# Performance work log

Hardware: AMD Instinct MI355X
Metric: run time of the kernel (lower is better)

## Reference

```python
import jax, jax.numpy as jnp
import numpy as np

N_NODES = 100000
N_EDGES = 1600000
D_IN = 256
H = 4       # n_heads
F = 64      # out_feats per head
NEG_SLOPE = 0.2


def setup_inputs() -> dict:
    key = jax.random.key(0)
    ks = jax.random.split(key, 8)
    feat = jax.random.normal(ks[0], (N_NODES, D_IN), dtype=jnp.float32)
    src = jax.random.randint(ks[1], (N_EDGES,), 0, N_NODES, dtype=jnp.int32)
    dst = jnp.sort(jax.random.randint(ks[2], (N_EDGES,), 0, N_NODES, dtype=jnp.int32))
    s = 1.0 / np.sqrt(D_IN)
    W_src = jax.random.normal(ks[3], (D_IN, H * F), dtype=jnp.float32) * s
    W_dst = jax.random.normal(ks[4], (D_IN, H * F), dtype=jnp.float32) * s
    b_dst = jnp.zeros((H * F,), dtype=jnp.float32)
    Wa_src = jax.random.normal(ks[5], (D_IN, H), dtype=jnp.float32) * s
    Wa_dst = jax.random.normal(ks[6], (D_IN, H), dtype=jnp.float32) * s
    return {"feat": feat, "W_src": W_src, "W_dst": W_dst, "b_dst": b_dst,
            "Wa_src": Wa_src, "Wa_dst": Wa_dst, "src": src, "dst": dst}


def reference(feat, W_src, W_dst, b_dst, Wa_src, Wa_dst, src, dst):
    N = feat.shape[0]
    # node projections
    h_src = (feat @ W_src).reshape(N, H, F)                  # [N,H,F]
    h_dst = (feat @ W_dst + b_dst).reshape(N, H, F)          # residual term
    a_src = feat @ Wa_src                                    # [N,H]
    a_dst = feat @ Wa_dst                                    # [N,H]
    # per-edge attention logits: u_add_v then leaky_relu
    e = a_src[src] + a_dst[dst]                              # [E,H]
    e = jnp.where(e > 0, e, NEG_SLOPE * e)
    # edge softmax grouped by destination node
    emax = jax.ops.segment_max(e, dst, num_segments=N)       # [N,H]
    emax = jnp.where(jnp.isfinite(emax), emax, 0.0)          # empty segments -> 0
    ex = jnp.exp(e - emax[dst])                              # [E,H]
    denom = jax.ops.segment_sum(ex, dst, num_segments=N)     # [N,H]
    a = ex / denom[dst]                                      # [E,H]
    # u_mul_e + sum aggregation
    msg = h_src[src] * a[:, :, None]                         # [E,H,F]
    out = jax.ops.segment_sum(msg, dst, num_segments=N)      # [N,H,F]
    return out + h_dst
```

## Files before the change

### kernel.cpp

```cpp
#include <hip/hip_runtime.h>

#define N_NODES 100000
#define N_EDGES 1600000
#define NEG_SLOPE 0.2f

typedef __bf16 bf16x8 __attribute__((ext_vector_type(8)));
typedef float f32x4 __attribute__((ext_vector_type(4)));

__device__ inline unsigned short f2bf(float f) {
    union { float f; unsigned u; } x; x.f = f;
    unsigned r = x.u + 0x7fffu + ((x.u >> 16) & 1u);
    return (unsigned short)(r >> 16);
}
__device__ inline float rlanef(float v, int l) {
    union { float f; int i; } x; x.f = v;
    x.i = __builtin_amdgcn_readlane(x.i, l);
    return x.f;
}

__global__ __launch_bounds__(256) void cvt_w_k(const float* __restrict__ Ws,
                                               const float* __restrict__ Wd,
                                               unsigned short* __restrict__ Wsw_src,
                                               unsigned short* __restrict__ Wsw_dst) {
    int idx = blockIdx.x * 256 + threadIdx.x;
    int sel = idx >> 16;
    int r = idx & 65535;
    int k = r >> 8, n = r & 255;
    int ct = n >> 4, nl = n & 15;
    int lane = ((k & 31) >> 3) * 16 + nl, j = k & 7;
    int ks = k >> 5;
    unsigned short v = f2bf((sel == 0 ? Ws : Wd)[k * 256 + n]);
    (sel == 0 ? Wsw_src : Wsw_dst)[(ct * 8 + ks) * 512 + lane * 8 + j] = v;
}

__global__ void cvt_wa_k(const float* __restrict__ Was,
                         const float* __restrict__ Wad,
                         unsigned short* __restrict__ Wa_sw) {
    int idx = blockIdx.x * 256 + threadIdx.x;
    int j = idx & 7, lane = (idx >> 3) & 63, ks = idx >> 9;
    int n = lane & 15, k = ks * 32 + (lane >> 4) * 8 + j;
    float v = n < 4 ? Was[k * 4 + n] : (n < 8 ? Wad[k * 4 + (n - 4)] : 0.f);
    Wa_sw[idx] = f2bf(v);
}

__global__ __launch_bounds__(256) void aproj_k(const float* __restrict__ feat,
                                               const unsigned short* __restrict__ Wa_sw,
                                               float* __restrict__ a_src,
                                               float* __restrict__ a_dst) {
    int wave = threadIdx.x >> 6, lane = threadIdx.x & 63;
    int quad = lane >> 4, l16 = lane & 15;
    int row_strip = (blockIdx.x * 4 + wave) * 16;
    int arow = row_strip + l16;
    if (arow >= N_NODES) arow = N_NODES - 1;
    const float* arow_p = feat + (size_t)arow * 256;
    const bf16x8* Wa8 = (const bf16x8*)Wa_sw;
    f32x4 acc = {0.f, 0.f, 0.f, 0.f};
    #pragma unroll
    for (int ks = 0; ks < 8; ++ks) {
        int k0 = ks * 32 + quad * 8;
        float4 f0 = *(const float4*)(arow_p + k0);
        float4 f1 = *(const float4*)(arow_p + k0 + 4);
        union { unsigned short u[8]; bf16x8 v; } cv;
        cv.u[0] = f2bf(f0.x); cv.u[1] = f2bf(f0.y);
        cv.u[2] = f2bf(f0.z); cv.u[3] = f2bf(f0.w);
        cv.u[4] = f2bf(f1.x); cv.u[5] = f2bf(f1.y);
        cv.u[6] = f2bf(f1.z); cv.u[7] = f2bf(f1.w);
        acc = __builtin_amdgcn_mfma_f32_16x16x32_bf16(cv.v, Wa8[ks * 64 + lane], acc, 0, 0, 0);
    }
    #pragma unroll
    for (int r = 0; r < 4; ++r) {
        int n = row_strip + quad * 4 + r;
        if (n < N_NODES) {
            if (l16 < 4)      a_src[n * 4 + l16] = acc[r];
            else if (l16 < 8) a_dst[n * 4 + (l16 - 4)] = acc[r];
        }
    }
}

__global__ void rowptr_k(const int* __restrict__ dst, int* __restrict__ rp) {
    int n = blockIdx.x * 256 + threadIdx.x;
    if (n > N_NODES) return;
    int lo = 0, hi = N_EDGES;
    while (lo < hi) { int mid = (lo + hi) >> 1; if (dst[mid] < n) lo = mid + 1; else hi = mid; }
    rp[n] = lo;
}

__global__ __launch_bounds__(512, 6) void agg_k(const int* __restrict__ src,
                                                const int* __restrict__ rp,
                                                const float* __restrict__ a_src,
                                                const float* __restrict__ a_dst,
                                                const float* __restrict__ feat,
                                                const unsigned short* __restrict__ Wsw_src,
                                                const unsigned short* __restrict__ Wsw_dst,
                                                const float* __restrict__ b_dst,
                                                float* __restrict__ out) {
    __shared__ unsigned short G[4 * 32 * 17 * 8];
    __shared__ unsigned short F[32 * 17 * 8];
    int tid = threadIdx.x, wave = tid >> 6, lane = tid & 63;
    int base = blockIdx.x * 16;

    #pragma unroll
    for (int e = tid; e < 1024; e += 512) {
        int m = e >> 6, k0 = (e & 63) * 4;
        float4 f = *(const float4*)(feat + (size_t)(base + m) * 256 + k0);
        ushort4 u;
        u.x = f2bf(f.x); u.y = f2bf(f.y); u.z = f2bf(f.z); u.w = f2bf(f.w);
        int ks = k0 >> 5, quad = (k0 >> 3) & 3, jb = k0 & 7;
        *(ushort4*)&F[((ks * 4 + quad) * 17 + m) * 8 + jb] = u;
    }

    for (int i = 0; i < 2; ++i) {
        int m = wave * 2 + i;
        int node = base + m;
        int r0 = rp[node], r1 = rp[node + 1];
        int deg = r1 - r0;
        f32x4 g0 = {0.f,0.f,0.f,0.f}, g1 = g0, g2 = g0, g3 = g0;

        if (deg > 0 && deg <= 64) {
            float4 adv = *(const float4*)(a_dst + node * 4);
            bool act = lane < deg;
            int s = 0;
            float4 av = {0.f, 0.f, 0.f, 0.f};
            if (act) {
                s = src[r0 + lane];
                av = *(const float4*)(a_src + s * 4);
            }
            float e0 = av.x + adv.x; e0 = e0 > 0.f ? e0 : NEG_SLOPE * e0;
            float e1 = av.y + adv.y; e1 = e1 > 0.f ? e1 : NEG_SLOPE * e1;
            float e2 = av.z + adv.z; e2 = e2 > 0.f ? e2 : NEG_SLOPE * e2;
            float e3 = av.w + adv.w; e3 = e3 > 0.f ? e3 : NEG_SLOPE * e3;
            if (!act) { e0 = e1 = e2 = e3 = -1e30f; }
            float m0 = e0, m1 = e1, m2 = e2, m3 = e3;
            #pragma unroll
            for (int off = 32; off > 0; off >>= 1) {
                m0 = fmaxf(m0, __shfl_xor(m0, off));
                m1 = fmaxf(m1, __shfl_xor(m1, off));
                m2 = fmaxf(m2, __shfl_xor(m2, off));
                m3 = fmaxf(m3, __shfl_xor(m3, off));
            }
            float w0 = act ? __expf(e0 - m0) : 0.f;
            float w1 = act ? __expf(e1 - m1) : 0.f;
            float w2 = act ? __expf(e2 - m2) : 0.f;
            float w3 = act ? __expf(e3 - m3) : 0.f;
            float d0 = w0, d1 = w1, d2 = w2, d3 = w3;
            #pragma unroll
            for (int off = 32; off > 0; off >>= 1) {
                d0 += __shfl_xor(d0, off); d1 += __shfl_xor(d1, off);
                d2 += __shfl_xor(d2, off); d3 += __shfl_xor(d3, off);
            }
            w0 *= 1.f / d0; w1 *= 1.f / d1; w2 *= 1.f / d2; w3 *= 1.f / d3;
            int j = 0;
            for (; j + 4 <= deg; j += 4) {
                int s0 = __builtin_amdgcn_readlane(s, j);
                int s1 = __builtin_amdgcn_readlane(s, j + 1);
                int s2 = __builtin_amdgcn_readlane(s, j + 2);
                int s3 = __builtin_amdgcn_readlane(s, j + 3);
                f32x4 f0 = *(const f32x4*)(feat + (size_t)s0 * 256 + lane * 4);
                f32x4 f1 = *(const f32x4*)(feat + (size_t)s1 * 256 + lane * 4);
                f32x4 f2 = *(const f32x4*)(feat + (size_t)s2 * 256 + lane * 4);
                f32x4 f3 = *(const f32x4*)(feat + (size_t)s3 * 256 + lane * 4);
                float a0 = rlanef(w0, j),   b0 = rlanef(w1, j),   c0 = rlanef(w2, j),   x0 = rlanef(w3, j);
                float a1 = rlanef(w0, j+1), b1 = rlanef(w1, j+1), c1 = rlanef(w2, j+1), x1 = rlanef(w3, j+1);
                float a2 = rlanef(w0, j+2), b2 = rlanef(w1, j+2), c2 = rlanef(w2, j+2), x2 = rlanef(w3, j+2);
                float a3 = rlanef(w0, j+3), b3 = rlanef(w1, j+3), c3 = rlanef(w2, j+3), x3 = rlanef(w3, j+3);
                g0 += a0 * f0; g1 += b0 * f0; g2 += c0 * f0; g3 += x0 * f0;
                g0 += a1 * f1; g1 += b1 * f1; g2 += c1 * f1; g3 += x1 * f1;
                g0 += a2 * f2; g1 += b2 * f2; g2 += c2 * f2; g3 += x2 * f2;
                g0 += a3 * f3; g1 += b3 * f3; g2 += c3 * f3; g3 += x3 * f3;
            }
            for (; j < deg; ++j) {
                int sj   = __builtin_amdgcn_readlane(s, j);
                float wx = rlanef(w0, j), wy = rlanef(w1, j);
                float wz = rlanef(w2, j), ww = rlanef(w3, j);
                f32x4 f = *(const f32x4*)(feat + (size_t)sj * 256 + lane * 4);
                g0 += wx * f; g1 += wy * f; g2 += wz * f; g3 += ww * f;
            }
        } else if (deg > 64) {
            float4 adv = *(const float4*)(a_dst + node * 4);
            float m0 = -1e30f, m1 = -1e30f, m2 = -1e30f, m3 = -1e30f;
            for (int e = r0 + lane; e < r1; e += 64) {
                int s = src[e];
                float4 av = *(const float4*)(a_src + s * 4);
                float e0 = av.x + adv.x; e0 = e0 > 0.f ? e0 : NEG_SLOPE * e0;
                float e1 = av.y + adv.y; e1 = e1 > 0.f ? e1 : NEG_SLOPE * e1;
                float e2 = av.z + adv.z; e2 = e2 > 0.f ? e2 : NEG_SLOPE * e2;
                float e3 = av.w + adv.w; e3 = e3 > 0.f ? e3 : NEG_SLOPE * e3;
                m0 = fmaxf(m0, e0); m1 = fmaxf(m1, e1);
                m2 = fmaxf(m2, e2); m3 = fmaxf(m3, e3);
            }
            #pragma unroll
            for (int off = 32; off > 0; off >>= 1) {
                m0 = fmaxf(m0, __shfl_xor(m0, off));
                m1 = fmaxf(m1, __shfl_xor(m1, off));
                m2 = fmaxf(m2, __shfl_xor(m2, off));
                m3 = fmaxf(m3, __shfl_xor(m3, off));
            }
            float d0 = 0.f, d1 = 0.f, d2 = 0.f, d3 = 0.f;
            for (int e = r0 + lane; e < r1; e += 64) {
                int s = src[e];
                float4 av = *(const float4*)(a_src + s * 4);
                float e0 = av.x + adv.x; e0 = e0 > 0.f ? e0 : NEG_SLOPE * e0;
                float e1 = av.y + adv.y; e1 = e1 > 0.f ? e1 : NEG_SLOPE * e1;
                float e2 = av.z + adv.z; e2 = e2 > 0.f ? e2 : NEG_SLOPE * e2;
                float e3 = av.w + adv.w; e3 = e3 > 0.f ? e3 : NEG_SLOPE * e3;
                d0 += __expf(e0 - m0); d1 += __expf(e1 - m1);
                d2 += __expf(e2 - m2); d3 += __expf(e3 - m3);
            }
            #pragma unroll
            for (int off = 32; off > 0; off >>= 1) {
                d0 += __shfl_xor(d0, off); d1 += __shfl_xor(d1, off);
                d2 += __shfl_xor(d2, off); d3 += __shfl_xor(d3, off);
            }
            float i0 = 1.f / d0, i1 = 1.f / d1, i2 = 1.f / d2, i3 = 1.f / d3;
            for (int c0 = r0; c0 < r1; c0 += 64) {
                int cnt = min(64, r1 - c0);
                int s = 0; float w0 = 0.f, w1 = 0.f, w2 = 0.f, w3 = 0.f;
                if (lane < cnt) {
                    s = src[c0 + lane];
                    float4 av = *(const float4*)(a_src + s * 4);
                    float e0 = av.x + adv.x; e0 = e0 > 0.f ? e0 : NEG_SLOPE * e0;
                    float e1 = av.y + adv.y; e1 = e1 > 0.f ? e1 : NEG_SLOPE * e1;
                    float e2 = av.z + adv.z; e2 = e2 > 0.f ? e2 : NEG_SLOPE * e2;
                    float e3 = av.w + adv.w; e3 = e3 > 0.f ? e3 : NEG_SLOPE * e3;
                    w0 = __expf(e0 - m0) * i0; w1 = __expf(e1 - m1) * i1;
                    w2 = __expf(e2 - m2) * i2; w3 = __expf(e3 - m3) * i3;
                }
                for (int j = 0; j < cnt; ++j) {
                    int sj   = __builtin_amdgcn_readlane(s, j);
                    float wx = rlanef(w0, j), wy = rlanef(w1, j);
                    float wz = rlanef(w2, j), ww = rlanef(w3, j);
                    f32x4 f = *(const f32x4*)(feat + (size_t)sj * 256 + lane * 4);
                    g0 += wx * f; g1 += wy * f; g2 += wz * f; g3 += ww * f;
                }
            }
        }

        int g8 = lane >> 1, off4 = (lane & 1) * 4;
        ushort4 u;
        u.x = f2bf(g0[0]); u.y = f2bf(g0[1]); u.z = f2bf(g0[2]); u.w = f2bf(g0[3]);
        *(ushort4*)&G[((0 * 32 + g8) * 17 + m) * 8 + off4] = u;
        u.x = f2bf(g1[0]); u.y = f2bf(g1[1]); u.z = f2bf(g1[2]); u.w = f2bf(g1[3]);
        *(ushort4*)&G[((1 * 32 + g8) * 17 + m) * 8 + off4] = u;
        u.x = f2bf(g2[0]); u.y = f2bf(g2[1]); u.z = f2bf(g2[2]); u.w = f2bf(g2[3]);
        *(ushort4*)&G[((2 * 32 + g8) * 17 + m) * 8 + off4] = u;
        u.x = f2bf(g3[0]); u.y = f2bf(g3[1]); u.z = f2bf(g3[2]); u.w = f2bf(g3[3]);
        *(ushort4*)&G[((3 * 32 + g8) * 17 + m) * 8 + off4] = u;
    }
    __syncthreads();

    int h = wave >> 1, hc = (wave & 1) * 2;
    int quad = lane >> 4, l16 = lane & 15;
    f32x4 acc[2];
    acc[0] = (f32x4){0.f, 0.f, 0.f, 0.f};
    acc[1] = (f32x4){0.f, 0.f, 0.f, 0.f};
    const bf16x8* Ws8 = (const bf16x8*)Wsw_src;
    const bf16x8* Wd8 = (const bf16x8*)Wsw_dst;
    #pragma unroll
    for (int ks = 0; ks < 8; ++ks) {
        bf16x8 a1 = *(const bf16x8*)&G[((h * 32 + ks * 4 + quad) * 17 + l16) * 8];
        bf16x8 a2 = *(const bf16x8*)&F[((ks * 4 + quad) * 17 + l16) * 8];
        #pragma unroll
        for (int c = 0; c < 2; ++c) {
            int ct = hc + c;
            acc[c] = __builtin_amdgcn_mfma_f32_16x16x32_bf16(
                a1, Ws8[((h * 4 + ct) * 8 + ks) * 64 + lane], acc[c], 0, 0, 0);
            acc[c] = __builtin_amdgcn_mfma_f32_16x16x32_bf16(
                a2, Wd8[((h * 4 + ct) * 8 + ks) * 64 + lane], acc[c], 0, 0, 0);
        }
    }
    #pragma unroll
    for (int c = 0; c < 2; ++c) {
        int col = h * 64 + (hc + c) * 16 + l16;
        float b = b_dst[col];
        #pragma unroll
        for (int r = 0; r < 4; ++r)
            out[(size_t)(base + quad * 4 + r) * 256 + col] = acc[c][r] + b;
    }
}

extern "C" void kernel_launch(void* const* d_in, const int* in_sizes, int n_in,
                              void* d_out, int out_size, void* d_ws, size_t ws_size,
                              hipStream_t stream) {
    const float* feat   = (const float*)d_in[0];
    const float* W_src  = (const float*)d_in[1];
    const float* W_dst  = (const float*)d_in[2];
    const float* b_dst  = (const float*)d_in[3];
    const float* Wa_src = (const float*)d_in[4];
    const float* Wa_dst = (const float*)d_in[5];
    const int*   src    = (const int*)d_in[6];
    const int*   dst    = (const int*)d_in[7];
    float* out = (float*)d_out;

    char* ws = (char*)d_ws;
    unsigned short* Wsw_src = (unsigned short*)(ws);
    unsigned short* Wsw_dst = (unsigned short*)(ws + 131072);
    unsigned short* Wa_sw   = (unsigned short*)(ws + 262144);
    float* a_src            = (float*)(ws + 270336);
    float* a_dst            = (float*)(ws + 1870336);
    int*   rp               = (int*)(ws + 3470336);

    hipLaunchKernelGGL(cvt_w_k,  dim3(512),  dim3(256), 0, stream, W_src, W_dst, Wsw_src, Wsw_dst);
    hipLaunchKernelGGL(cvt_wa_k, dim3(16),   dim3(256), 0, stream, Wa_src, Wa_dst, Wa_sw);
    hipLaunchKernelGGL(aproj_k,  dim3(1563), dim3(256), 0, stream, feat, Wa_sw, a_src, a_dst);
    hipLaunchKernelGGL(rowptr_k, dim3(391),  dim3(256), 0, stream, dst, rp);
    hipLaunchKernelGGL(agg_k,    dim3(6250), dim3(512), 0, stream, src, rp, a_src, a_dst,
                       feat, Wsw_src, Wsw_dst, b_dst, out);
}
```

Baseline: 469.6 us.

## Project features before aggregation and gather fp16 h_src instead of raw feat

Splits the fused gather-then-project kernel into a dense projection kernel, which writes h_src in fp16 and the h_dst+bias residual into out, followed by an aggregation kernel with one wave per node. Each edge now gathers 256 fp16 values (512 B) instead of 256 fp32 feat values (1 KB), and does a single weighted sum per lane rather than four per-head sums. Attention logits are stored as fp16, softmax weights are passed through shared memory instead of readlane, and the shuffle reductions stop once they cover the node's degree. The cost is an extra 51 MB round trip for h_src plus a read-modify-write of out, along with some precision loss from fp16 storage.

```diff
diff --git a/kernel.cpp b/kernel.cpp
--- a/kernel.cpp
+++ b/kernel.cpp
@@ -6,16 +6,12 @@
 
 typedef __bf16 bf16x8 __attribute__((ext_vector_type(8)));
 typedef float f32x4 __attribute__((ext_vector_type(4)));
+typedef _Float16 f16x4 __attribute__((ext_vector_type(4)));
 
 __device__ inline unsigned short f2bf(float f) {
     union { float f; unsigned u; } x; x.f = f;
     unsigned r = x.u + 0x7fffu + ((x.u >> 16) & 1u);
     return (unsigned short)(r >> 16);
-}
-__device__ inline float rlanef(float v, int l) {
-    union { float f; int i; } x; x.f = v;
-    x.i = __builtin_amdgcn_readlane(x.i, l);
-    return x.f;
 }
 
 __global__ __launch_bounds__(256) void cvt_w_k(const float* __restrict__ Ws,
@@ -43,10 +39,18 @@
     Wa_sw[idx] = f2bf(v);
 }
 
+__global__ void rowptr_k(const int* __restrict__ dst, int* __restrict__ rp) {
+    int n = blockIdx.x * 256 + threadIdx.x;
+    if (n > N_NODES) return;
+    int lo = 0, hi = N_EDGES;
+    while (lo < hi) { int mid = (lo + hi) >> 1; if (dst[mid] < n) lo = mid + 1; else hi = mid; }
+    rp[n] = lo;
+}
+
 __global__ __launch_bounds__(256) void aproj_k(const float* __restrict__ feat,
                                                const unsigned short* __restrict__ Wa_sw,
-                                               float* __restrict__ a_src,
-                                               float* __restrict__ a_dst) {
+                                               _Float16* __restrict__ a_srcH,
+                                               _Float16* __restrict__ a_dstH) {
     int wave = threadIdx.x >> 6, lane = threadIdx.x & 63;
     int quad = lane >> 4, l16 = lane & 15;
     int row_strip = (blockIdx.x * 4 + wave) * 16;
@@ -71,211 +75,241 @@
     for (int r = 0; r < 4; ++r) {
         int n = row_strip + quad * 4 + r;
         if (n < N_NODES) {
-            if (l16 < 4)      a_src[n * 4 + l16] = acc[r];
-            else if (l16 < 8) a_dst[n * 4 + (l16 - 4)] = acc[r];
-        }
-    }
-}
-
-__global__ void rowptr_k(const int* __restrict__ dst, int* __restrict__ rp) {
-    int n = blockIdx.x * 256 + threadIdx.x;
-    if (n > N_NODES) return;
-    int lo = 0, hi = N_EDGES;
-    while (lo < hi) { int mid = (lo + hi) >> 1; if (dst[mid] < n) lo = mid + 1; else hi = mid; }
-    rp[n] = lo;
-}
-
-__global__ __launch_bounds__(512, 6) void agg_k(const int* __restrict__ src,
-                                                const int* __restrict__ rp,
-                                                const float* __restrict__ a_src,
-                                                const float* __restrict__ a_dst,
-                                                const float* __restrict__ feat,
-                                                const unsigned short* __restrict__ Wsw_src,
-                                                const unsigned short* __restrict__ Wsw_dst,
-                                                const float* __restrict__ b_dst,
-                                                float* __restrict__ out) {
-    __shared__ unsigned short G[4 * 32 * 17 * 8];
-    __shared__ unsigned short F[32 * 17 * 8];
+            if (l16 < 4)      a_srcH[(size_t)n * 4 + l16] = (_Float16)acc[r];
+            else if (l16 < 8) a_dstH[(size_t)n * 4 + (l16 - 4)] = (_Float16)acc[r];
+        }
+    }
+}
+
+__global__ __launch_bounds__(512) void proj_k(const float* __restrict__ feat,
+                                              const unsigned short* __restrict__ Wsw_src,
+                                              const unsigned short* __restrict__ Wsw_dst,
+                                              const float* __restrict__ b_dst,
+                                              _Float16* __restrict__ h_src,
+                                              float* __restrict__ out) {
+    __shared__ unsigned short F[4 * 32 * 17 * 8];
     int tid = threadIdx.x, wave = tid >> 6, lane = tid & 63;
-    int base = blockIdx.x * 16;
-
-    #pragma unroll
-    for (int e = tid; e < 1024; e += 512) {
-        int m = e >> 6, k0 = (e & 63) * 4;
-        float4 f = *(const float4*)(feat + (size_t)(base + m) * 256 + k0);
+    int quad = lane >> 4, l16 = lane & 15;
+    int base = blockIdx.x * 64;
+
+    #pragma unroll
+    for (int it = 0; it < 8; ++it) {
+        int c = tid + it * 512;
+        int m = c >> 6, k0 = (c & 63) * 4;
+        int row = base + m; if (row > N_NODES - 1) row = N_NODES - 1;
+        float4 f = *(const float4*)(feat + (size_t)row * 256 + k0);
         ushort4 u;
         u.x = f2bf(f.x); u.y = f2bf(f.y); u.z = f2bf(f.z); u.w = f2bf(f.w);
-        int ks = k0 >> 5, quad = (k0 >> 3) & 3, jb = k0 & 7;
-        *(ushort4*)&F[((ks * 4 + quad) * 17 + m) * 8 + jb] = u;
-    }
-
-    for (int i = 0; i < 2; ++i) {
-        int m = wave * 2 + i;
-        int node = base + m;
-        int r0 = rp[node], r1 = rp[node + 1];
-        int deg = r1 - r0;
-        f32x4 g0 = {0.f,0.f,0.f,0.f}, g1 = g0, g2 = g0, g3 = g0;
-
-        if (deg > 0 && deg <= 64) {
-            float4 adv = *(const float4*)(a_dst + node * 4);
-            bool act = lane < deg;
-            int s = 0;
-            float4 av = {0.f, 0.f, 0.f, 0.f};
-            if (act) {
-                s = src[r0 + lane];
-                av = *(const float4*)(a_src + s * 4);
-            }
-            float e0 = av.x + adv.x; e0 = e0 > 0.f ? e0 : NEG_SLOPE * e0;
-            float e1 = av.y + adv.y; e1 = e1 > 0.f ? e1 : NEG_SLOPE * e1;
-            float e2 = av.z + adv.z; e2 = e2 > 0.f ? e2 : NEG_SLOPE * e2;
-            float e3 = av.w + adv.w; e3 = e3 > 0.f ? e3 : NEG_SLOPE * e3;
-            if (!act) { e0 = e1 = e2 = e3 = -1e30f; }
-            float m0 = e0, m1 = e1, m2 = e2, m3 = e3;
+        int strip = m >> 4, ms = m & 15, kq = k0 >> 3, jb = k0 & 7;
+        *(ushort4*)&F[((strip * 32 + kq) * 17 + ms) * 8 + jb] = u;
+    }
+    __syncthreads();
+
+    bool isSrc = wave < 4;
+    int cg = (wave & 3) * 4;
+    const bf16x8* W8 = (const bf16x8*)(isSrc ? Wsw_src : Wsw_dst);
+
+    f32x4 acc[4][4];
+    #pragma unroll
+    for (int s = 0; s < 4; ++s)
+        #pragma unroll
+        for (int c = 0; c < 4; ++c) acc[s][c] = (f32x4){0.f, 0.f, 0.f, 0.f};
+
+    #pragma unroll
+    for (int ks = 0; ks < 8; ++ks) {
+        bf16x8 B0 = W8[((cg + 0) * 8 + ks) * 64 + lane];
+        bf16x8 B1 = W8[((cg + 1) * 8 + ks) * 64 + lane];
+        bf16x8 B2 = W8[((cg + 2) * 8 + ks) * 64 + lane];
+        bf16x8 B3 = W8[((cg + 3) * 8 + ks) * 64 + lane];
+        #pragma unroll
+        for (int s = 0; s < 4; ++s) {
+            bf16x8 A = *(const bf16x8*)&F[((s * 32 + ks * 4 + quad) * 17 + l16) * 8];
+            acc[s][0] = __builtin_amdgcn_mfma_f32_16x16x32_bf16(A, B0, acc[s][0], 0, 0, 0);
+            acc[s][1] = __builtin_amdgcn_mfma_f32_16x16x32_bf16(A, B1, acc[s][1], 0, 0, 0);
+            acc[s][2] = __builtin_amdgcn_mfma_f32_16x16x32_bf16(A, B2, acc[s][2], 0, 0, 0);
+            acc[s][3] = __builtin_amdgcn_mfma_f32_16x16x32_bf16(A, B3, acc[s][3], 0, 0, 0);
+        }
+    }
+
+    if (isSrc) {
+        #pragma unroll
+        for (int s = 0; s < 4; ++s)
             #pragma unroll
-            for (int off = 32; off > 0; off >>= 1) {
-                m0 = fmaxf(m0, __shfl_xor(m0, off));
-                m1 = fmaxf(m1, __shfl_xor(m1, off));
-                m2 = fmaxf(m2, __shfl_xor(m2, off));
-                m3 = fmaxf(m3, __shfl_xor(m3, off));
-            }
-            float w0 = act ? __expf(e0 - m0) : 0.f;
-            float w1 = act ? __expf(e1 - m1) : 0.f;
-            float w2 = act ? __expf(e2 - m2) : 0.f;
-            float w3 = act ? __expf(e3 - m3) : 0.f;
-            float d0 = w0, d1 = w1, d2 = w2, d3 = w3;
-            #pragma unroll
-            for (int off = 32; off > 0; off >>= 1) {
-                d0 += __shfl_xor(d0, off); d1 += __shfl_xor(d1, off);
-                d2 += __shfl_xor(d2, off); d3 += __shfl_xor(d3, off);
-            }
-            w0 *= 1.f / d0; w1 *= 1.f / d1; w2 *= 1.f / d2; w3 *= 1.f / d3;
-            int j = 0;
-            for (; j + 4 <= deg; j += 4) {
-                int s0 = __builtin_amdgcn_readlane(s, j);
-                int s1 = __builtin_amdgcn_readlane(s, j + 1);
-                int s2 = __builtin_amdgcn_readlane(s, j + 2);
-                int s3 = __builtin_amdgcn_readlane(s, j + 3);
-                f32x4 f0 = *(const f32x4*)(feat + (size_t)s0 * 256 + lane * 4);
-                f32x4 f1 = *(const f32x4*)(feat + (size_t)s1 * 256 + lane * 4);
-                f32x4 f2 = *(const f32x4*)(feat + (size_t)s2 * 256 + lane * 4);
-                f32x4 f3 = *(const f32x4*)(feat + (size_t)s3 * 256 + lane * 4);
-                float a0 = rlanef(w0, j),   b0 = rlanef(w1, j),   c0 = rlanef(w2, j),   x0 = rlanef(w3, j);
-                float a1 = rlanef(w0, j+1), b1 = rlanef(w1, j+1), c1 = rlanef(w2, j+1), x1 = rlanef(w3, j+1);
-                float a2 = rlanef(w0, j+2), b2 = rlanef(w1, j+2), c2 = rlanef(w2, j+2), x2 = rlanef(w3, j+2);
-                float a3 = rlanef(w0, j+3), b3 = rlanef(w1, j+3), c3 = rlanef(w2, j+3), x3 = rlanef(w3, j+3);
-                g0 += a0 * f0; g1 += b0 * f0; g2 += c0 * f0; g3 += x0 * f0;
-                g0 += a1 * f1; g1 += b1 * f1; g2 += c1 * f1; g3 += x1 * f1;
-                g0 += a2 * f2; g1 += b2 * f2; g2 += c2 * f2; g3 += x2 * f2;
-                g0 += a3 * f3; g1 += b3 * f3; g2 += c3 * f3; g3 += x3 * f3;
-            }
-            for (; j < deg; ++j) {
-                int sj   = __builtin_amdgcn_readlane(s, j);
-                float wx = rlanef(w0, j), wy = rlanef(w1, j);
-                float wz = rlanef(w2, j), ww = rlanef(w3, j);
-                f32x4 f = *(const f32x4*)(feat + (size_t)sj * 256 + lane * 4);
-                g0 += wx * f; g1 += wy * f; g2 += wz * f; g3 += ww * f;
-            }
-        } else if (deg > 64) {
-            float4 adv = *(const float4*)(a_dst + node * 4);
-            float m0 = -1e30f, m1 = -1e30f, m2 = -1e30f, m3 = -1e30f;
-            for (int e = r0 + lane; e < r1; e += 64) {
-                int s = src[e];
-                float4 av = *(const float4*)(a_src + s * 4);
-                float e0 = av.x + adv.x; e0 = e0 > 0.f ? e0 : NEG_SLOPE * e0;
-                float e1 = av.y + adv.y; e1 = e1 > 0.f ? e1 : NEG_SLOPE * e1;
-                float e2 = av.z + adv.z; e2 = e2 > 0.f ? e2 : NEG_SLOPE * e2;
-                float e3 = av.w + adv.w; e3 = e3 > 0.f ? e3 : NEG_SLOPE * e3;
-                m0 = fmaxf(m0, e0); m1 = fmaxf(m1, e1);
-                m2 = fmaxf(m2, e2); m3 = fmaxf(m3, e3);
-            }
-            #pragma unroll
-            for (int off = 32; off > 0; off >>= 1) {
-                m0 = fmaxf(m0, __shfl_xor(m0, off));
-                m1 = fmaxf(m1, __shfl_xor(m1, off));
-                m2 = fmaxf(m2, __shfl_xor(m2, off));
-                m3 = fmaxf(m3, __shfl_xor(m3, off));
-            }
-            float d0 = 0.f, d1 = 0.f, d2 = 0.f, d3 = 0.f;
-            for (int e = r0 + lane; e < r1; e += 64) {
-                int s = src[e];
-                float4 av = *(const float4*)(a_src + s * 4);
-                float e0 = av.x + adv.x; e0 = e0 > 0.f ? e0 : NEG_SLOPE * e0;
-                float e1 = av.y + adv.y; e1 = e1 > 0.f ? e1 : NEG_SLOPE * e1;
-                float e2 = av.z + adv.z; e2 = e2 > 0.f ? e2 : NEG_SLOPE * e2;
-                float e3 = av.w + adv.w; e3 = e3 > 0.f ? e3 : NEG_SLOPE * e3;
-                d0 += __expf(e0 - m0); d1 += __expf(e1 - m1);
-                d2 += __expf(e2 - m2); d3 += __expf(e3 - m3);
-            }
-            #pragma unroll
-            for (int off = 32; off > 0; off >>= 1) {
-                d0 += __shfl_xor(d0, off); d1 += __shfl_xor(d1, off);
-                d2 += __shfl_xor(d2, off); d3 += __shfl_xor(d3, off);
-            }
-            float i0 = 1.f / d0, i1 = 1.f / d1, i2 = 1.f / d2, i3 = 1.f / d3;
-            for (int c0 = r0; c0 < r1; c0 += 64) {
-                int cnt = min(64, r1 - c0);
-                int s = 0; float w0 = 0.f, w1 = 0.f, w2 = 0.f, w3 = 0.f;
-                if (lane < cnt) {
-                    s = src[c0 + lane];
-                    float4 av = *(const float4*)(a_src + s * 4);
-                    float e0 = av.x + adv.x; e0 = e0 > 0.f ? e0 : NEG_SLOPE * e0;
-                    float e1 = av.y + adv.y; e1 = e1 > 0.f ? e1 : NEG_SLOPE * e1;
-                    float e2 = av.z + adv.z; e2 = e2 > 0.f ? e2 : NEG_SLOPE * e2;
-                    float e3 = av.w + adv.w; e3 = e3 > 0.f ? e3 : NEG_SLOPE * e3;
-                    w0 = __expf(e0 - m0) * i0; w1 = __expf(e1 - m1) * i1;
-                    w2 = __expf(e2 - m2) * i2; w3 = __expf(e3 - m3) * i3;
-                }
-                for (int j = 0; j < cnt; ++j) {
-                    int sj   = __builtin_amdgcn_readlane(s, j);
-                    float wx = rlanef(w0, j), wy = rlanef(w1, j);
-                    float wz = rlanef(w2, j), ww = rlanef(w3, j);
-                    f32x4 f = *(const f32x4*)(feat + (size_t)sj * 256 + lane * 4);
-                    g0 += wx * f; g1 += wy * f; g2 += wz * f; g3 += ww * f;
+            for (int c = 0; c < 4; ++c) {
+                int col = (cg + c) * 16 + l16;
+                #pragma unroll
+                for (int r = 0; r < 4; ++r) {
+                    int row = base + s * 16 + quad * 4 + r;
+                    if (row < N_NODES)
+                        h_src[(size_t)row * 256 + col] = (_Float16)acc[s][c][r];
                 }
             }
-        }
-
-        int g8 = lane >> 1, off4 = (lane & 1) * 4;
-        ushort4 u;
-        u.x = f2bf(g0[0]); u.y = f2bf(g0[1]); u.z = f2bf(g0[2]); u.w = f2bf(g0[3]);
-        *(ushort4*)&G[((0 * 32 + g8) * 17 + m) * 8 + off4] = u;
-        u.x = f2bf(g1[0]); u.y = f2bf(g1[1]); u.z = f2bf(g1[2]); u.w = f2bf(g1[3]);
-        *(ushort4*)&G[((1 * 32 + g8) * 17 + m) * 8 + off4] = u;
-        u.x = f2bf(g2[0]); u.y = f2bf(g2[1]); u.z = f2bf(g2[2]); u.w = f2bf(g2[3]);
-        *(ushort4*)&G[((2 * 32 + g8) * 17 + m) * 8 + off4] = u;
-        u.x = f2bf(g3[0]); u.y = f2bf(g3[1]); u.z = f2bf(g3[2]); u.w = f2bf(g3[3]);
-        *(ushort4*)&G[((3 * 32 + g8) * 17 + m) * 8 + off4] = u;
-    }
-    __syncthreads();
-
-    int h = wave >> 1, hc = (wave & 1) * 2;
-    int quad = lane >> 4, l16 = lane & 15;
-    f32x4 acc[2];
-    acc[0] = (f32x4){0.f, 0.f, 0.f, 0.f};
-    acc[1] = (f32x4){0.f, 0.f, 0.f, 0.f};
-    const bf16x8* Ws8 = (const bf16x8*)Wsw_src;
-    const bf16x8* Wd8 = (const bf16x8*)Wsw_dst;
-    #pragma unroll
-    for (int ks = 0; ks < 8; ++ks) {
-        bf16x8 a1 = *(const bf16x8*)&G[((h * 32 + ks * 4 + quad) * 17 + l16) * 8];
-        bf16x8 a2 = *(const bf16x8*)&F[((ks * 4 + quad) * 17 + l16) * 8];
-        #pragma unroll
-        for (int c = 0; c < 2; ++c) {
-            int ct = hc + c;
-            acc[c] = __builtin_amdgcn_mfma_f32_16x16x32_bf16(
-                a1, Ws8[((h * 4 + ct) * 8 + ks) * 64 + lane], acc[c], 0, 0, 0);
-            acc[c] = __builtin_amdgcn_mfma_f32_16x16x32_bf16(
-                a2, Wd8[((h * 4 + ct) * 8 + ks) * 64 + lane], acc[c], 0, 0, 0);
-        }
-    }
-    #pragma unroll
-    for (int c = 0; c < 2; ++c) {
-        int col = h * 64 + (hc + c) * 16 + l16;
-        float b = b_dst[col];
-        #pragma unroll
-        for (int r = 0; r < 4; ++r)
-            out[(size_t)(base + quad * 4 + r) * 256 + col] = acc[c][r] + b;
-    }
+    } else {
+        #pragma unroll
+        for (int c = 0; c < 4; ++c) {
+            int col = (cg + c) * 16 + l16;
+            float b = b_dst[col];
+            #pragma unroll
+            for (int s = 0; s < 4; ++s)
+                #pragma unroll
+                for (int r = 0; r < 4; ++r) {
+                    int row = base + s * 16 + quad * 4 + r;
+                    if (row < N_NODES)
+                        out[(size_t)row * 256 + col] = acc[s][c][r] + b;
+                }
+        }
+    }
+}
+
+__global__ __launch_bounds__(256, 6) void agg2_k(const int* __restrict__ src,
+                                                 const int* __restrict__ rp,
+                                                 const _Float16* __restrict__ a_srcH,
+                                                 const _Float16* __restrict__ a_dstH,
+                                                 const _Float16* __restrict__ h_src,
+                                                 float* __restrict__ out) {
+    __shared__ float WT[4][64][4];
+    int tid = threadIdx.x, wave = tid >> 6, lane = tid & 63;
+    int node = blockIdx.x * 4 + wave;
+    int head = lane >> 4;
+    int r0 = rp[node], r1 = rp[node + 1], deg = r1 - r0;
+
+    size_t o = (size_t)node * 256 + lane * 4;
+    float4 pv = *(const float4*)(out + o);
+
+    f32x4 g = (f32x4){0.f, 0.f, 0.f, 0.f};
+    const _Float16* hl = h_src + lane * 4;
+
+    if (deg > 0 && deg <= 64) {
+        f16x4 adv4 = *(const f16x4*)(a_dstH + (size_t)node * 4);
+        float ad0 = (float)adv4[0], ad1 = (float)adv4[1];
+        float ad2 = (float)adv4[2], ad3 = (float)adv4[3];
+        bool act = lane < deg;
+        int s = 0;
+        f16x4 av4 = (f16x4){0, 0, 0, 0};
+        if (act) {
+            s = src[r0 + lane];
+            av4 = *(const f16x4*)(a_srcH + (size_t)s * 4);
+        }
+        float e0 = (float)av4[0] + ad0; e0 = e0 > 0.f ? e0 : NEG_SLOPE * e0;
+        float e1 = (float)av4[1] + ad1; e1 = e1 > 0.f ? e1 : NEG_SLOPE * e1;
+        float e2 = (float)av4[2] + ad2; e2 = e2 > 0.f ? e2 : NEG_SLOPE * e2;
+        float e3 = (float)av4[3] + ad3; e3 = e3 > 0.f ? e3 : NEG_SLOPE * e3;
+        if (!act) { e0 = e1 = e2 = e3 = -1e30f; }
+        float m0 = e0, m1 = e1, m2 = e2, m3 = e3;
+        for (int off = 1; off < deg; off <<= 1) {
+            m0 = fmaxf(m0, __shfl_xor(m0, off));
+            m1 = fmaxf(m1, __shfl_xor(m1, off));
+            m2 = fmaxf(m2, __shfl_xor(m2, off));
+            m3 = fmaxf(m3, __shfl_xor(m3, off));
+        }
+        float w0 = act ? __expf(e0 - m0) : 0.f;
+        float w1 = act ? __expf(e1 - m1) : 0.f;
+        float w2 = act ? __expf(e2 - m2) : 0.f;
+        float w3 = act ? __expf(e3 - m3) : 0.f;
+        float d0 = w0, d1 = w1, d2 = w2, d3 = w3;
+        for (int off = 1; off < deg; off <<= 1) {
+            d0 += __shfl_xor(d0, off); d1 += __shfl_xor(d1, off);
+            d2 += __shfl_xor(d2, off); d3 += __shfl_xor(d3, off);
+        }
+        w0 *= 1.f / d0; w1 *= 1.f / d1; w2 *= 1.f / d2; w3 *= 1.f / d3;
+        float4 wv; wv.x = w0; wv.y = w1; wv.z = w2; wv.w = w3;
+        *(float4*)&WT[wave][lane][0] = wv;
+        asm volatile("s_waitcnt lgkmcnt(0)" ::: "memory");
+
+        int j = 0;
+        for (; j + 4 <= deg; j += 4) {
+            int s0 = __builtin_amdgcn_readlane(s, j);
+            int s1 = __builtin_amdgcn_readlane(s, j + 1);
+            int s2 = __builtin_amdgcn_readlane(s, j + 2);
+            int s3 = __builtin_amdgcn_readlane(s, j + 3);
+            f16x4 h0 = *(const f16x4*)(hl + (size_t)s0 * 256);
+            f16x4 h1 = *(const f16x4*)(hl + (size_t)s1 * 256);
+            f16x4 h2 = *(const f16x4*)(hl + (size_t)s2 * 256);
+            f16x4 h3 = *(const f16x4*)(hl + (size_t)s3 * 256);
+            float x0 = WT[wave][j][head],     x1 = WT[wave][j + 1][head];
+            float x2 = WT[wave][j + 2][head], x3 = WT[wave][j + 3][head];
+            g[0] += x0 * (float)h0[0]; g[1] += x0 * (float)h0[1];
+            g[2] += x0 * (float)h0[2]; g[3] += x0 * (float)h0[3];
+            g[0] += x1 * (float)h1[0]; g[1] += x1 * (float)h1[1];
+            g[2] += x1 * (float)h1[2]; g[3] += x1 * (float)h1[3];
+            g[0] += x2 * (float)h2[0]; g[1] += x2 * (float)h2[1];
+            g[2] += x2 * (float)h2[2]; g[3] += x2 * (float)h2[3];
+            g[0] += x3 * (float)h3[0]; g[1] += x3 * (float)h3[1];
+            g[2] += x3 * (float)h3[2]; g[3] += x3 * (float)h3[3];
+        }
+        for (; j < deg; ++j) {
+            int sj = __builtin_amdgcn_readlane(s, j);
+            float xj = WT[wave][j][head];
+            f16x4 h = *(const f16x4*)(hl + (size_t)sj * 256);
+            g[0] += xj * (float)h[0]; g[1] += xj * (float)h[1];
+            g[2] += xj * (float)h[2]; g[3] += xj * (float)h[3];
+        }
+    } else if (deg > 64) {
+        f16x4 adv4 = *(const f16x4*)(a_dstH + (size_t)node * 4);
+        float ad0 = (float)adv4[0], ad1 = (float)adv4[1];
+        float ad2 = (float)adv4[2], ad3 = (float)adv4[3];
+        float m0 = -1e30f, m1 = -1e30f, m2 = -1e30f, m3 = -1e30f;
+        for (int e = r0 + lane; e < r1; e += 64) {
+            int se = src[e];
+            f16x4 av4 = *(const f16x4*)(a_srcH + (size_t)se * 4);
+            float e0 = (float)av4[0] + ad0; e0 = e0 > 0.f ? e0 : NEG_SLOPE * e0;
+            float e1 = (float)av4[1] + ad1; e1 = e1 > 0.f ? e1 : NEG_SLOPE * e1;
+            float e2 = (float)av4[2] + ad2; e2 = e2 > 0.f ? e2 : NEG_SLOPE * e2;
+            float e3 = (float)av4[3] + ad3; e3 = e3 > 0.f ? e3 : NEG_SLOPE * e3;
+            m0 = fmaxf(m0, e0); m1 = fmaxf(m1, e1);
+            m2 = fmaxf(m2, e2); m3 = fmaxf(m3, e3);
+        }
+        #pragma unroll
+        for (int off = 32; off > 0; off >>= 1) {
+            m0 = fmaxf(m0, __shfl_xor(m0, off)); m1 = fmaxf(m1, __shfl_xor(m1, off));
+            m2 = fmaxf(m2, __shfl_xor(m2, off)); m3 = fmaxf(m3, __shfl_xor(m3, off));
+        }
+        float d0 = 0.f, d1 = 0.f, d2 = 0.f, d3 = 0.f;
+        for (int e = r0 + lane; e < r1; e += 64) {
+            int se = src[e];
+            f16x4 av4 = *(const f16x4*)(a_srcH + (size_t)se * 4);
+            float e0 = (float)av4[0] + ad0; e0 = e0 > 0.f ? e0 : NEG_SLOPE * e0;
+            float e1 = (float)av4[1] + ad1; e1 = e1 > 0.f ? e1 : NEG_SLOPE * e1;
+            float e2 = (float)av4[2] + ad2; e2 = e2 > 0.f ? e2 : NEG_SLOPE * e2;
+            float e3 = (float)av4[3] + ad3; e3 = e3 > 0.f ? e3 : NEG_SLOPE * e3;
+            d0 += __expf(e0 - m0); d1 += __expf(e1 - m1);
+            d2 += __expf(e2 - m2); d3 += __expf(e3 - m3);
+        }
+        #pragma unroll
+        for (int off = 32; off > 0; off >>= 1) {
+            d0 += __shfl_xor(d0, off); d1 += __shfl_xor(d1, off);
+            d2 += __shfl_xor(d2, off); d3 += __shfl_xor(d3, off);
+        }
+        float i0 = 1.f / d0, i1 = 1.f / d1, i2 = 1.f / d2, i3 = 1.f / d3;
+        for (int c0 = r0; c0 < r1; c0 += 64) {
+            int cnt = min(64, r1 - c0);
+            int s = 0; float w0 = 0.f, w1 = 0.f, w2 = 0.f, w3 = 0.f;
+            if (lane < cnt) {
+                s = src[c0 + lane];
+                f16x4 av4 = *(const f16x4*)(a_srcH + (size_t)s * 4);
+                float e0 = (float)av4[0] + ad0; e0 = e0 > 0.f ? e0 : NEG_SLOPE * e0;
+                float e1 = (float)av4[1] + ad1; e1 = e1 > 0.f ? e1 : NEG_SLOPE * e1;
+                float e2 = (float)av4[2] + ad2; e2 = e2 > 0.f ? e2 : NEG_SLOPE * e2;
+                float e3 = (float)av4[3] + ad3; e3 = e3 > 0.f ? e3 : NEG_SLOPE * e3;
+                w0 = __expf(e0 - m0) * i0; w1 = __expf(e1 - m1) * i1;
+                w2 = __expf(e2 - m2) * i2; w3 = __expf(e3 - m3) * i3;
+            }
+            float4 wv; wv.x = w0; wv.y = w1; wv.z = w2; wv.w = w3;
+            *(float4*)&WT[wave][lane][0] = wv;
+            asm volatile("s_waitcnt lgkmcnt(0)" ::: "memory");
+            for (int j = 0; j < cnt; ++j) {
+                int sj = __builtin_amdgcn_readlane(s, j);
+                float xj = WT[wave][j][head];
+                f16x4 h = *(const f16x4*)(hl + (size_t)sj * 256);
+                g[0] += xj * (float)h[0]; g[1] += xj * (float)h[1];
+                g[2] += xj * (float)h[2]; g[3] += xj * (float)h[3];
+            }
+        }
+    }
+    float4 res;
+    res.x = pv.x + g[0]; res.y = pv.y + g[1];
+    res.z = pv.z + g[2]; res.w = pv.w + g[3];
+    *(float4*)(out + o) = res;
 }
 
 extern "C" void kernel_launch(void* const* d_in, const int* in_sizes, int n_in,
@@ -290,19 +324,22 @@
     const int*   src    = (const int*)d_in[6];
     const int*   dst    = (const int*)d_in[7];
     float* out = (float*)d_out;
-
     char* ws = (char*)d_ws;
-    unsigned short* Wsw_src = (unsigned short*)(ws);
-    unsigned short* Wsw_dst = (unsigned short*)(ws + 131072);
-    unsigned short* Wa_sw   = (unsigned short*)(ws + 262144);
-    float* a_src            = (float*)(ws + 270336);
-    float* a_dst            = (float*)(ws + 1870336);
-    int*   rp               = (int*)(ws + 3470336);
-
-    hipLaunchKernelGGL(cvt_w_k,  dim3(512),  dim3(256), 0, stream, W_src, W_dst, Wsw_src, Wsw_dst);
-    hipLaunchKernelGGL(cvt_wa_k, dim3(16),   dim3(256), 0, stream, Wa_src, Wa_dst, Wa_sw);
-    hipLaunchKernelGGL(aproj_k,  dim3(1563), dim3(256), 0, stream, feat, Wa_sw, a_src, a_dst);
-    hipLaunchKernelGGL(rowptr_k, dim3(391),  dim3(256), 0, stream, dst, rp);
-    hipLaunchKernelGGL(agg_k,    dim3(6250), dim3(512), 0, stream, src, rp, a_src, a_dst,
-                       feat, Wsw_src, Wsw_dst, b_dst, out);
-}
+
+    _Float16* h_srcH        = (_Float16*)(ws);
+    unsigned short* Wsw_src = (unsigned short*)(ws + 51200000);
+    unsigned short* Wsw_dst = (unsigned short*)(ws + 51331072);
+    unsigned short* Wa_sw   = (unsigned short*)(ws + 51462144);
+    _Float16* a_srcH        = (_Float16*)(ws + 51470336);
+    _Float16* a_dstH        = (_Float16*)(ws + 52270336);
+    int*      rp            = (int*)(ws + 53070336);
+
+    hipLaunchKernelGGL(cvt_w_k,  dim3(512),   dim3(256), 0, stream, W_src, W_dst, Wsw_src, Wsw_dst);
+    hipLaunchKernelGGL(cvt_wa_k, dim3(16),    dim3(256), 0, stream, Wa_src, Wa_dst, Wa_sw);
+    hipLaunchKernelGGL(rowptr_k, dim3(391),   dim3(256), 0, stream, dst, rp);
+    hipLaunchKernelGGL(aproj_k,  dim3(1563),  dim3(256), 0, stream, feat, Wa_sw, a_srcH, a_dstH);
+    hipLaunchKernelGGL(proj_k,   dim3(1563),  dim3(512), 0, stream, feat, Wsw_src, Wsw_dst,
+                       b_dst, h_srcH, out);
+    hipLaunchKernelGGL(agg2_k,   dim3(25000), dim3(256), 0, stream, src, rp, a_srcH, a_dstH,
+                       h_srcH, out);
+}
```

After: 419.3 us. 1.12x faster.
